# Kernel tuning notes

Measured on AMD Instinct MI355X. Metric: run time of the kernel, lower is better.

Reference implementation:

```python
import jax, jax.numpy as jnp
import numpy as np

CLASSES = 11  # log2 tile values 0..10
B = 262144


def setup_inputs() -> dict:
    key = jax.random.key(0)
    k1, k2, k3 = jax.random.split(key, 3)
    # boards: 0 (empty) or powers of 2 up to 2^10, per the 2048 game / classes=11
    e = jax.random.randint(k1, (B, 4, 4), 0, CLASSES)
    x = jnp.where(e == 0, 0.0, jnp.exp2(e.astype(jnp.float32)))
    W0 = jax.random.normal(k2, (4, CLASSES + 1, 1, 2), dtype=jnp.float32) * 0.1
    b0 = jnp.full((4,), 0.01, dtype=jnp.float32)
    W1 = jax.random.normal(k3, (4, CLASSES + 1, 2, 1), dtype=jnp.float32) * 0.1
    return {"x": x, "W0": W0, "b0": b0, "W1": W1}


def _preprocess(x):
    # x: [B,4,4] raw tile values
    corners = jnp.stack([x[:, 0, 0], x[:, 0, -1], x[:, -1, 0], x[:, -1, -1]], axis=1)
    ix = jnp.argmax(corners, axis=1)
    fv = (ix // 2) == 1  # vertical flip (rows)
    fh = (ix % 2) == 1   # horizontal flip (cols)
    x = jnp.where(fv[:, None, None], x[:, ::-1, :], x)
    x = jnp.where(fh[:, None, None], x[:, :, ::-1], x)
    xlog = jnp.log2(x + (x == 0)).astype(jnp.int32)           # [B,4,4] in 0..10
    onehot = jax.nn.one_hot(xlog, CLASSES, dtype=jnp.float32)  # [B,4,4,11]
    out = jnp.transpose(onehot, (0, 3, 1, 2))                  # [B,11,4,4]
    mask = out.sum(axis=1, keepdims=True)                      # occupancy mask
    out = jnp.concatenate([mask, out], axis=1)                 # [B,12,4,4]
    # unscramble: undo flip-dependent channel ordering (vert swaps 0<->1, horiz swaps 2<->3)
    perm_v = jnp.array([1, 0, 2, 3, 4, 5, 6, 7, 8, 9, 10, 11])
    perm_h = jnp.array([0, 1, 3, 2, 4, 5, 6, 7, 8, 9, 10, 11])
    out = jnp.where(fv[:, None, None, None], out[:, perm_v], out)
    out = jnp.where(fh[:, None, None, None], out[:, perm_h], out)
    return out


def _conv(x, W):
    return jax.lax.conv_general_dilated(
        x, W, window_strides=(1, 1), padding='VALID',
        dimension_numbers=('NCHW', 'OIHW', 'NCHW'))


def reference(x, W0, b0, W1):
    p = _preprocess(x)                                   # [B,12,4,4]
    zh = jax.nn.relu(_conv(p, W0) + b0[None, :, None, None])  # [B,4,4,3]
    zv = jax.nn.relu(_conv(p, W1))                             # [B,4,3,4]
    # transpose zv so the horizontal/vertical feature maps can be stacked
    return jnp.stack((zh, jnp.transpose(zv, (0, 1, 3, 2))), axis=1)  # [B,2,4,4,3]
```

## Files before the change

kernel.cpp:

```cpp
#include <hip/hip_runtime.h>


__global__ __launch_bounds__(256) void smartcnn_kernel(
    const float* __restrict__ x,
    const float* __restrict__ W0,
    const float* __restrict__ b0,
    const float* __restrict__ W1,
    float* __restrict__ out,
    int B)
{
    __shared__ float tab0h[176], tab1h[176];
    __shared__ float tab0v[176], tab1v[176];
    __shared__ float sC0[16], sC1[16];

    const int t = threadIdx.x;
    if (t < 176) {
        int flip = t / 44, rem = t % 44, o = rem / 11, e = rem % 11;
        int fvv = flip >> 1, fhh = flip & 1;
        int ch;
        if (e == 0)      ch = fvv ? 0 : 1;
        else if (e == 1) ch = fhh ? 3 : 2;
        else if (e == 2) ch = fhh ? 2 : 3;
        else             ch = 1 + e;
        tab0h[t] = W0[o * 24 + ch * 2 + 0];
        tab1h[t] = W0[o * 24 + ch * 2 + 1];
        tab0v[t] = W1[o * 24 + ch * 2 + 0];
        tab1v[t] = W1[o * 24 + ch * 2 + 1];
    }
    if (t < 16) {
        int flip = t >> 2, o = t & 3, mcf = (flip >> 1) & 1;
        sC0[t] = b0[o] + W0[o * 24 + mcf * 2] + W0[o * 24 + mcf * 2 + 1];
        sC1[t] =          W1[o * 24 + mcf * 2] + W1[o * 24 + mcf * 2 + 1];
    }
    __syncthreads();

    int gq = blockIdx.x * 256 + t;
    int b = gq >> 2;
    int q = gq & 3;
    if (b >= B) return;

    const float4* x4 = (const float4*)x + (size_t)b * 4;
    float4 r0 = x4[0], r1 = x4[1], r2 = x4[2], r3 = x4[3];

    float best = r0.x; int ix = 0;
    if (r0.w > best) { best = r0.w; ix = 1; }
    if (r3.x > best) { best = r3.x; ix = 2; }
    if (r3.w > best) { best = r3.w; ix = 3; }
    const int flipsel = ix;
    const int fv = ix >> 1, fh = ix & 1;
    const int M  = fv * 12 + fh * 3;
    const int fb = flipsel * 44;

#define EVAL(v) (max((int)(__float_as_uint(v) >> 23) - 127, 0))
    unsigned pack0 = (unsigned)EVAL(r0.x)        | ((unsigned)EVAL(r0.y) << 4)  |
                     ((unsigned)EVAL(r0.z) << 8)  | ((unsigned)EVAL(r0.w) << 12) |
                     ((unsigned)EVAL(r1.x) << 16) | ((unsigned)EVAL(r1.y) << 20) |
                     ((unsigned)EVAL(r1.z) << 24) | ((unsigned)EVAL(r1.w) << 28);
    unsigned pack1 = (unsigned)EVAL(r2.x)        | ((unsigned)EVAL(r2.y) << 4)  |
                     ((unsigned)EVAL(r2.z) << 8)  | ((unsigned)EVAL(r2.w) << 12) |
                     ((unsigned)EVAL(r3.x) << 16) | ((unsigned)EVAL(r3.y) << 20) |
                     ((unsigned)EVAL(r3.z) << 24) | ((unsigned)EVAL(r3.w) << 28);
#undef EVAL

#define EX(c) (int)(((c) < 8 ? pack0 : pack1) >> (((c) & 7) * 4) & 15u)

    float4* out4 = (float4*)out + (size_t)b * 24;

#pragma unroll
    for (int rp = 0; rp < 3; ++rp) {
        const int n  = rp * 4 + q;
        const int o  = (n * 11) >> 5;
        const int s  = n - 3 * o;
        const int f1 = (s == 2) ? 1 : 0;
        const int f2 = (s >= 1) ? 1 : 0;
        const int s5 = s * 5;
        const int base = fb + o * 11;

        {
            const float Ch = sC0[flipsel * 4 + o];
            int c0 = s5, c1 = s5 + 1 + f1, c2 = s5 + 2 + f2, c3 = s5 + 4;
            float4 val;
            val.x = fmaxf(Ch + tab0h[base + EX(c0 ^ M)] + tab1h[base + EX((c0 + 1) ^ M)], 0.f);
            val.y = fmaxf(Ch + tab0h[base + EX(c1 ^ M)] + tab1h[base + EX((c1 + 1) ^ M)], 0.f);
            val.z = fmaxf(Ch + tab0h[base + EX(c2 ^ M)] + tab1h[base + EX((c2 + 1) ^ M)], 0.f);
            val.w = fmaxf(Ch + tab0h[base + EX(c3 ^ M)] + tab1h[base + EX((c3 + 1) ^ M)], 0.f);
            out4[rp * 4 + q] = val;
        }
        {
            const float Cv = sC1[flipsel * 4 + o];
            int c0 = s5, c1 = s5 + 4 - 11 * f1, c2 = s5 + 8 - 11 * f2, c3 = s5 + 1;
            float4 val;
            val.x = fmaxf(Cv + tab0v[base + EX(c0 ^ M)] + tab1v[base + EX((c0 + 4) ^ M)], 0.f);
            val.y = fmaxf(Cv + tab0v[base + EX(c1 ^ M)] + tab1v[base + EX((c1 + 4) ^ M)], 0.f);
            val.z = fmaxf(Cv + tab0v[base + EX(c2 ^ M)] + tab1v[base + EX((c2 + 4) ^ M)], 0.f);
            val.w = fmaxf(Cv + tab0v[base + EX(c3 ^ M)] + tab1v[base + EX((c3 + 4) ^ M)], 0.f);
            out4[12 + rp * 4 + q] = val;
        }
    }
#undef EX
}

extern "C" void kernel_launch(void* const* d_in, const int* in_sizes, int n_in,
                              void* d_out, int out_size, void* d_ws, size_t ws_size,
                              hipStream_t stream) {
    const float* x  = (const float*)d_in[0];
    const float* W0 = (const float*)d_in[1];
    const float* b0 = (const float*)d_in[2];
    const float* W1 = (const float*)d_in[3];
    float* out = (float*)d_out;

    int B = in_sizes[0] / 16;
    int total = B * 4;
    int blocks = (total + 255) / 256;
    smartcnn_kernel<<<blocks, 256, 0, stream>>>(x, W0, b0, W1, out, B);
}
```

Before: 24.35 us.

## Precompute pairwise ReLU lookup tables and share board rows via shuffles

```diff
diff --git a/kernel.cpp b/kernel.cpp
--- a/kernel.cpp
+++ b/kernel.cpp
@@ -1,7 +1,14 @@
 #include <hip/hip_runtime.h>
 
 
-__global__ __launch_bounds__(256) void smartcnn_kernel(
+__device__ __forceinline__ int chmap(int e, int fv, int fh) {
+    if (e == 0) return fv ? 0 : 1;
+    if (e == 1) return fh ? 3 : 2;
+    if (e == 2) return fh ? 2 : 3;
+    return 1 + e;
+}
+
+__global__ __launch_bounds__(1024) void smartcnn_kernel(
     const float* __restrict__ x,
     const float* __restrict__ W0,
     const float* __restrict__ b0,
@@ -9,93 +16,103 @@
     float* __restrict__ out,
     int B)
 {
-    __shared__ float tab0h[176], tab1h[176];
-    __shared__ float tab0v[176], tab1v[176];
-    __shared__ float sC0[16], sC1[16];
+    __shared__ float tabH[1936];
+    __shared__ float tabV[1936];
+    __shared__ float sW0[96], sW1[96], sb0[4];
 
     const int t = threadIdx.x;
-    if (t < 176) {
-        int flip = t / 44, rem = t % 44, o = rem / 11, e = rem % 11;
-        int fvv = flip >> 1, fhh = flip & 1;
-        int ch;
-        if (e == 0)      ch = fvv ? 0 : 1;
-        else if (e == 1) ch = fhh ? 3 : 2;
-        else if (e == 2) ch = fhh ? 2 : 3;
-        else             ch = 1 + e;
-        tab0h[t] = W0[o * 24 + ch * 2 + 0];
-        tab1h[t] = W0[o * 24 + ch * 2 + 1];
-        tab0v[t] = W1[o * 24 + ch * 2 + 0];
-        tab1v[t] = W1[o * 24 + ch * 2 + 1];
-    }
-    if (t < 16) {
-        int flip = t >> 2, o = t & 3, mcf = (flip >> 1) & 1;
-        sC0[t] = b0[o] + W0[o * 24 + mcf * 2] + W0[o * 24 + mcf * 2 + 1];
-        sC1[t] =          W1[o * 24 + mcf * 2] + W1[o * 24 + mcf * 2 + 1];
+    if (t < 96) { sW0[t] = W0[t]; sW1[t] = W1[t]; }
+    if (t < 4)  sb0[t] = b0[t];
+    __syncthreads();
+
+#pragma unroll
+    for (int it = 0; it < 2; ++it) {
+        int id = t + it * 1024;
+        if (id < 1936) {
+            int e2 = id % 11;
+            int r  = id / 11;
+            int e1 = r % 11;
+            int fo = r / 11;
+            int o = fo & 3, flip = fo >> 2;
+            int fvv = flip >> 1, fhh = flip & 1;
+            int ch1 = chmap(e1, fvv, fhh);
+            int ch2 = chmap(e2, fvv, fhh);
+            int mc2 = fvv ? 2 : 0;
+            int o24 = o * 24;
+            float C0 = sb0[o] + sW0[o24 + mc2] + sW0[o24 + mc2 + 1];
+            float C1 =          sW1[o24 + mc2] + sW1[o24 + mc2 + 1];
+            tabH[id] = fmaxf(C0 + sW0[o24 + ch1 * 2] + sW0[o24 + ch2 * 2 + 1], 0.0f);
+            tabV[id] = fmaxf(C1 + sW1[o24 + ch1 * 2] + sW1[o24 + ch2 * 2 + 1], 0.0f);
+        }
     }
     __syncthreads();
 
-    int gq = blockIdx.x * 256 + t;
-    int b = gq >> 2;
-    int q = gq & 3;
+    const int gq = blockIdx.x * 1024 + t;
+    const int b = gq >> 2;
+    const int q = gq & 3;
     if (b >= B) return;
 
-    const float4* x4 = (const float4*)x + (size_t)b * 4;
-    float4 r0 = x4[0], r1 = x4[1], r2 = x4[2], r3 = x4[3];
+    float4 row = ((const float4*)x)[(size_t)b * 4 + q];
 
-    float best = r0.x; int ix = 0;
-    if (r0.w > best) { best = r0.w; ix = 1; }
-    if (r3.x > best) { best = r3.x; ix = 2; }
-    if (r3.w > best) { best = r3.w; ix = 3; }
-    const int flipsel = ix;
+#define EV(v) (max((int)(__float_as_uint(v) >> 23) - 127, 0))
+    unsigned my = (unsigned)EV(row.x)        | ((unsigned)EV(row.y) << 4) |
+                  ((unsigned)EV(row.z) << 8) | ((unsigned)EV(row.w) << 12);
+#undef EV
+    unsigned oth1 = __shfl_xor(my, 1);
+    unsigned pair = (q & 1) ? ((my << 16) | oth1) : ((oth1 << 16) | my);
+    unsigned oth2 = __shfl_xor(pair, 2);
+    unsigned pk0 = (q & 2) ? oth2 : pair;
+    unsigned pk1 = (q & 2) ? pair : oth2;
+
+    int e00 = pk0 & 15, e03 = (pk0 >> 12) & 15;
+    int e30 = (pk1 >> 16) & 15, e33 = (int)(pk1 >> 28);
+    int best = e00, ix = 0;
+    if (e03 > best) { best = e03; ix = 1; }
+    if (e30 > best) { best = e30; ix = 2; }
+    if (e33 > best) { best = e33; ix = 3; }
     const int fv = ix >> 1, fh = ix & 1;
-    const int M  = fv * 12 + fh * 3;
-    const int fb = flipsel * 44;
 
-#define EVAL(v) (max((int)(__float_as_uint(v) >> 23) - 127, 0))
-    unsigned pack0 = (unsigned)EVAL(r0.x)        | ((unsigned)EVAL(r0.y) << 4)  |
-                     ((unsigned)EVAL(r0.z) << 8)  | ((unsigned)EVAL(r0.w) << 12) |
-                     ((unsigned)EVAL(r1.x) << 16) | ((unsigned)EVAL(r1.y) << 20) |
-                     ((unsigned)EVAL(r1.z) << 24) | ((unsigned)EVAL(r1.w) << 28);
-    unsigned pack1 = (unsigned)EVAL(r2.x)        | ((unsigned)EVAL(r2.y) << 4)  |
-                     ((unsigned)EVAL(r2.z) << 8)  | ((unsigned)EVAL(r2.w) << 12) |
-                     ((unsigned)EVAL(r3.x) << 16) | ((unsigned)EVAL(r3.y) << 20) |
-                     ((unsigned)EVAL(r3.z) << 24) | ((unsigned)EVAL(r3.w) << 28);
-#undef EVAL
+    unsigned fva = (pk1 >> 16) | (pk1 << 16);
+    unsigned fvb = (pk0 >> 16) | (pk0 << 16);
+    pk0 = fv ? fva : pk0;
+    pk1 = fv ? fvb : pk1;
+    unsigned ra = ((pk0 & 0x0F0F0F0Fu) << 4) | ((pk0 >> 4) & 0x0F0F0F0Fu);
+    ra = ((ra & 0x00FF00FFu) << 8) | ((ra >> 8) & 0x00FF00FFu);
+    unsigned rb = ((pk1 & 0x0F0F0F0Fu) << 4) | ((pk1 >> 4) & 0x0F0F0F0Fu);
+    rb = ((rb & 0x00FF00FFu) << 8) | ((rb >> 8) & 0x00FF00FFu);
+    pk0 = fh ? ra : pk0;
+    pk1 = fh ? rb : pk1;
 
-#define EX(c) (int)(((c) < 8 ? pack0 : pack1) >> (((c) & 7) * 4) & 15u)
+    const unsigned long long pk = ((unsigned long long)pk1 << 32) | (unsigned long long)pk0;
+#define EX(c) ((int)((pk >> ((c) * 4)) & 15ull))
 
     float4* out4 = (float4*)out + (size_t)b * 24;
 
 #pragma unroll
     for (int rp = 0; rp < 3; ++rp) {
-        const int n  = rp * 4 + q;
-        const int o  = (n * 11) >> 5;
-        const int s  = n - 3 * o;
-        const int f1 = (s == 2) ? 1 : 0;
-        const int f2 = (s >= 1) ? 1 : 0;
-        const int s5 = s * 5;
-        const int base = fb + o * 11;
+        int n = rp * 4 + q;
+        int o = (n * 11) >> 5;
+        int s = n - 3 * o;
+        int f1 = (s == 2) ? 1 : 0;
+        int f2 = (s >= 1) ? 1 : 0;
+        int s5 = s * 5;
+        int base = (ix * 4 + o) * 121;
 
-        {
-            const float Ch = sC0[flipsel * 4 + o];
-            int c0 = s5, c1 = s5 + 1 + f1, c2 = s5 + 2 + f2, c3 = s5 + 4;
-            float4 val;
-            val.x = fmaxf(Ch + tab0h[base + EX(c0 ^ M)] + tab1h[base + EX((c0 + 1) ^ M)], 0.f);
-            val.y = fmaxf(Ch + tab0h[base + EX(c1 ^ M)] + tab1h[base + EX((c1 + 1) ^ M)], 0.f);
-            val.z = fmaxf(Ch + tab0h[base + EX(c2 ^ M)] + tab1h[base + EX((c2 + 1) ^ M)], 0.f);
-            val.w = fmaxf(Ch + tab0h[base + EX(c3 ^ M)] + tab1h[base + EX((c3 + 1) ^ M)], 0.f);
-            out4[rp * 4 + q] = val;
-        }
-        {
-            const float Cv = sC1[flipsel * 4 + o];
-            int c0 = s5, c1 = s5 + 4 - 11 * f1, c2 = s5 + 8 - 11 * f2, c3 = s5 + 1;
-            float4 val;
-            val.x = fmaxf(Cv + tab0v[base + EX(c0 ^ M)] + tab1v[base + EX((c0 + 4) ^ M)], 0.f);
-            val.y = fmaxf(Cv + tab0v[base + EX(c1 ^ M)] + tab1v[base + EX((c1 + 4) ^ M)], 0.f);
-            val.z = fmaxf(Cv + tab0v[base + EX(c2 ^ M)] + tab1v[base + EX((c2 + 4) ^ M)], 0.f);
-            val.w = fmaxf(Cv + tab0v[base + EX(c3 ^ M)] + tab1v[base + EX((c3 + 4) ^ M)], 0.f);
-            out4[12 + rp * 4 + q] = val;
-        }
+        int c0 = s5, c1 = s5 + 1 + f1, c2 = s5 + 2 + f2, c3 = s5 + 4;
+        float4 vh;
+        vh.x = tabH[base + EX(c0) * 11 + EX(c0 + 1)];
+        vh.y = tabH[base + EX(c1) * 11 + EX(c1 + 1)];
+        vh.z = tabH[base + EX(c2) * 11 + EX(c2 + 1)];
+        vh.w = tabH[base + EX(c3) * 11 + EX(c3 + 1)];
+        out4[rp * 4 + q] = vh;
+
+        int d0 = s5, d1 = s5 + 4 - 11 * f1, d2 = s5 + 8 - 11 * f2, d3 = s5 + 1;
+        float4 vv;
+        vv.x = tabV[base + EX(d0) * 11 + EX(d0 + 4)];
+        vv.y = tabV[base + EX(d1) * 11 + EX(d1 + 4)];
+        vv.z = tabV[base + EX(d2) * 11 + EX(d2 + 4)];
+        vv.w = tabV[base + EX(d3) * 11 + EX(d3 + 4)];
+        out4[12 + rp * 4 + q] = vv;
     }
 #undef EX
 }
@@ -111,6 +128,6 @@
 
     int B = in_sizes[0] / 16;
     int total = B * 4;
-    int blocks = (total + 255) / 256;
-    smartcnn_kernel<<<blocks, 256, 0, stream>>>(x, W0, b0, W1, out, B);
+    int blocks = (total + 1023) / 1024;
+    smartcnn_kernel<<<blocks, 1024, 0, stream>>>(x, W0, b0, W1, out, B);
 }
```

After: 25.01 us. +2.7%, slower.

## Assign one output float4 per thread instead of six per thread

Applied to the files above, without the earlier changes.

```diff
diff --git a/kernel.cpp b/kernel.cpp
--- a/kernel.cpp
+++ b/kernel.cpp
@@ -9,9 +9,8 @@
     float* __restrict__ out,
     int B)
 {
-    __shared__ float tab0h[176], tab1h[176];
-    __shared__ float tab0v[176], tab1v[176];
-    __shared__ float sC0[16], sC1[16];
+    __shared__ float tabs[704];
+    __shared__ float sC[32];
 
     const int t = threadIdx.x;
     if (t < 176) {
@@ -22,22 +21,26 @@
         else if (e == 1) ch = fhh ? 3 : 2;
         else if (e == 2) ch = fhh ? 2 : 3;
         else             ch = 1 + e;
-        tab0h[t] = W0[o * 24 + ch * 2 + 0];
-        tab1h[t] = W0[o * 24 + ch * 2 + 1];
-        tab0v[t] = W1[o * 24 + ch * 2 + 0];
-        tab1v[t] = W1[o * 24 + ch * 2 + 1];
+        tabs[t]       = W0[o * 24 + ch * 2 + 0];
+        tabs[176 + t] = W0[o * 24 + ch * 2 + 1];
+        tabs[352 + t] = W1[o * 24 + ch * 2 + 0];
+        tabs[528 + t] = W1[o * 24 + ch * 2 + 1];
     }
-    if (t < 16) {
-        int flip = t >> 2, o = t & 3, mcf = (flip >> 1) & 1;
-        sC0[t] = b0[o] + W0[o * 24 + mcf * 2] + W0[o * 24 + mcf * 2 + 1];
-        sC1[t] =          W1[o * 24 + mcf * 2] + W1[o * 24 + mcf * 2 + 1];
+    if (t < 32) {
+        int half = t >> 4, flip = (t >> 2) & 3, o = t & 3;
+        int mcf = (flip >> 1) & 1;
+        const float* W = half ? W1 : W0;
+        float c = W[o * 24 + mcf * 2] + W[o * 24 + mcf * 2 + 1];
+        if (!half) c += b0[o];
+        sC[t] = c;
     }
     __syncthreads();
 
-    int gq = blockIdx.x * 256 + t;
-    int b = gq >> 2;
-    int q = gq & 3;
-    if (b >= B) return;
+    const int f = blockIdx.x * 256 + t;
+    if (f >= B * 24) return;
+
+    const int b = (int)((unsigned)f / 24u);
+    const int slot = f - b * 24;
 
     const float4* x4 = (const float4*)x + (size_t)b * 4;
     float4 r0 = x4[0], r1 = x4[1], r2 = x4[2], r3 = x4[3];
@@ -46,58 +49,50 @@
     if (r0.w > best) { best = r0.w; ix = 1; }
     if (r3.x > best) { best = r3.x; ix = 2; }
     if (r3.w > best) { best = r3.w; ix = 3; }
-    const int flipsel = ix;
     const int fv = ix >> 1, fh = ix & 1;
     const int M  = fv * 12 + fh * 3;
-    const int fb = flipsel * 44;
+    const int fb = ix * 44;
 
 #define EVAL(v) (max((int)(__float_as_uint(v) >> 23) - 127, 0))
-    unsigned pack0 = (unsigned)EVAL(r0.x)        | ((unsigned)EVAL(r0.y) << 4)  |
-                     ((unsigned)EVAL(r0.z) << 8)  | ((unsigned)EVAL(r0.w) << 12) |
-                     ((unsigned)EVAL(r1.x) << 16) | ((unsigned)EVAL(r1.y) << 20) |
-                     ((unsigned)EVAL(r1.z) << 24) | ((unsigned)EVAL(r1.w) << 28);
-    unsigned pack1 = (unsigned)EVAL(r2.x)        | ((unsigned)EVAL(r2.y) << 4)  |
-                     ((unsigned)EVAL(r2.z) << 8)  | ((unsigned)EVAL(r2.w) << 12) |
-                     ((unsigned)EVAL(r3.x) << 16) | ((unsigned)EVAL(r3.y) << 20) |
-                     ((unsigned)EVAL(r3.z) << 24) | ((unsigned)EVAL(r3.w) << 28);
+    unsigned pk0 = (unsigned)EVAL(r0.x)        | ((unsigned)EVAL(r0.y) << 4)  |
+                   ((unsigned)EVAL(r0.z) << 8)  | ((unsigned)EVAL(r0.w) << 12) |
+                   ((unsigned)EVAL(r1.x) << 16) | ((unsigned)EVAL(r1.y) << 20) |
+                   ((unsigned)EVAL(r1.z) << 24) | ((unsigned)EVAL(r1.w) << 28);
+    unsigned pk1 = (unsigned)EVAL(r2.x)        | ((unsigned)EVAL(r2.y) << 4)  |
+                   ((unsigned)EVAL(r2.z) << 8)  | ((unsigned)EVAL(r2.w) << 12) |
+                   ((unsigned)EVAL(r3.x) << 16) | ((unsigned)EVAL(r3.y) << 20) |
+                   ((unsigned)EVAL(r3.z) << 24) | ((unsigned)EVAL(r3.w) << 28);
 #undef EVAL
+    const unsigned long long pk =
+        ((unsigned long long)pk1 << 32) | (unsigned long long)pk0;
+#define EX(c) ((int)((pk >> ((((c) ^ M) * 4))) & 15ull))
 
-#define EX(c) (int)(((c) < 8 ? pack0 : pack1) >> (((c) & 7) * 4) & 15u)
+    const int half = slot >= 12;
+    const int n  = half ? slot - 12 : slot;
+    const int o  = (n * 11) >> 5;
+    const int s  = n - 3 * o;
+    const int f1 = (s == 2) ? 1 : 0;
+    const int f2 = (s >= 1) ? 1 : 0;
+    const int s5 = s * 5;
 
-    float4* out4 = (float4*)out + (size_t)b * 24;
+    const int c0 = s5;
+    const int c1 = half ? s5 + 4 - 11 * f1 : s5 + 1 + f1;
+    const int c2 = half ? s5 + 8 - 11 * f2 : s5 + 2 + f2;
+    const int c3 = half ? s5 + 1           : s5 + 4;
+    const int p  = half ? 4 : 1;
 
-#pragma unroll
-    for (int rp = 0; rp < 3; ++rp) {
-        const int n  = rp * 4 + q;
-        const int o  = (n * 11) >> 5;
-        const int s  = n - 3 * o;
-        const int f1 = (s == 2) ? 1 : 0;
-        const int f2 = (s >= 1) ? 1 : 0;
-        const int s5 = s * 5;
-        const int base = fb + o * 11;
+    const int base0 = half * 352 + fb + o * 11;
+    const int base1 = base0 + 176;
+    const float C = sC[half * 16 + ix * 4 + o];
 
-        {
-            const float Ch = sC0[flipsel * 4 + o];
-            int c0 = s5, c1 = s5 + 1 + f1, c2 = s5 + 2 + f2, c3 = s5 + 4;
-            float4 val;
-            val.x = fmaxf(Ch + tab0h[base + EX(c0 ^ M)] + tab1h[base + EX((c0 + 1) ^ M)], 0.f);
-            val.y = fmaxf(Ch + tab0h[base + EX(c1 ^ M)] + tab1h[base + EX((c1 + 1) ^ M)], 0.f);
-            val.z = fmaxf(Ch + tab0h[base + EX(c2 ^ M)] + tab1h[base + EX((c2 + 1) ^ M)], 0.f);
-            val.w = fmaxf(Ch + tab0h[base + EX(c3 ^ M)] + tab1h[base + EX((c3 + 1) ^ M)], 0.f);
-            out4[rp * 4 + q] = val;
-        }
-        {
-            const float Cv = sC1[flipsel * 4 + o];
-            int c0 = s5, c1 = s5 + 4 - 11 * f1, c2 = s5 + 8 - 11 * f2, c3 = s5 + 1;
-            float4 val;
-            val.x = fmaxf(Cv + tab0v[base + EX(c0 ^ M)] + tab1v[base + EX((c0 + 4) ^ M)], 0.f);
-            val.y = fmaxf(Cv + tab0v[base + EX(c1 ^ M)] + tab1v[base + EX((c1 + 4) ^ M)], 0.f);
-            val.z = fmaxf(Cv + tab0v[base + EX(c2 ^ M)] + tab1v[base + EX((c2 + 4) ^ M)], 0.f);
-            val.w = fmaxf(Cv + tab0v[base + EX(c3 ^ M)] + tab1v[base + EX((c3 + 4) ^ M)], 0.f);
-            out4[12 + rp * 4 + q] = val;
-        }
-    }
+    float4 val;
+    val.x = fmaxf(C + tabs[base0 + EX(c0)] + tabs[base1 + EX(c0 + p)], 0.f);
+    val.y = fmaxf(C + tabs[base0 + EX(c1)] + tabs[base1 + EX(c1 + p)], 0.f);
+    val.z = fmaxf(C + tabs[base0 + EX(c2)] + tabs[base1 + EX(c2 + p)], 0.f);
+    val.w = fmaxf(C + tabs[base0 + EX(c3)] + tabs[base1 + EX(c3 + p)], 0.f);
 #undef EX
+
+    ((float4*)out)[f] = val;
 }
 
 extern "C" void kernel_launch(void* const* d_in, const int* in_sizes, int n_in,
@@ -110,7 +105,7 @@
     float* out = (float*)d_out;
 
     int B = in_sizes[0] / 16;
-    int total = B * 4;
+    int total = B * 24;
     int blocks = (total + 255) / 256;
     smartcnn_kernel<<<blocks, 256, 0, stream>>>(x, W0, b0, W1, out, B);
 }
```

Result: slower. 42.74 us (+75.5%).
